# Performance work log

Measured on AMD Instinct MI355X. Metric: run time of the kernel, lower is better.

## Reference

```python
import jax, jax.numpy as jnp
import numpy as np


def setup_inputs() -> dict:
    key = jax.random.key(0)
    k1, k2, k3 = jax.random.split(key, 3)
    B, C, S, Fin, Fout = 16, 64, 2048, 64, 64
    x = jax.random.normal(k1, (B, C, S, Fin), dtype=jnp.float32)
    # positive entries so row sums are > 0 and sqrt is well-defined
    adj = jax.random.uniform(k2, (C, C), dtype=jnp.float32)
    weight = jax.random.normal(k3, (Fin, Fout), dtype=jnp.float32) * (1.0 / np.sqrt(Fin))
    return {"x": x, "adj": adj, "weight": weight}


def reference(x, adj, weight):
    # Symmetric normalization: D^{-1/2} A D^{-1/2}. The torch code builds a
    # full diag + matrix inverse; mathematically this is elementwise rsqrt
    # row/col scaling of adj.
    d_inv_sqrt = jax.lax.rsqrt(jnp.sum(adj, axis=1))          # [C]
    norm_adj = adj * d_inv_sqrt[:, None] * d_inv_sqrt[None, :]  # [C, C]
    # support[b,c,s,o] = sum_f x[b,c,s,f] * weight[f,o]
    support = jnp.einsum('bcsf,fo->bcso', x, weight)
    # mix over channel (graph node) dim: out[b,c,s,o] = sum_d A_norm[c,d] support[b,d,s,o]
    out = jnp.einsum('cd,bdso->bcso', norm_adj, support)
    return jax.nn.relu(out)
```

## Files before the change

kernel.cpp:

```cpp
#include <hip/hip_runtime.h>
#include <hip/hip_bf16.h>

#define B_ 16
#define C_ 64
#define S_ 2048
#define F_ 64
#define SF (S_ * F_)

typedef __attribute__((ext_vector_type(8))) short short8;
typedef __attribute__((ext_vector_type(4))) float float4_;

#define SWZ(row, col) ((col) ^ (((row) & 7) << 3))

__device__ __forceinline__ unsigned short f2bf(float f) {
    unsigned int u = __builtin_bit_cast(unsigned int, f);
    u += 0x7fffu + ((u >> 16) & 1u);
    return (unsigned short)(u >> 16);
}

__global__ void gcn_prep(const float* __restrict__ adj, const float* __restrict__ wgt,
                         unsigned short* __restrict__ nadj, unsigned short* __restrict__ wT)
{
    __shared__ float dis[C_];
    const int t = threadIdx.x;
    if (t < C_) {
        float s = 0.f;
        for (int d = 0; d < C_; ++d) s += adj[t * C_ + d];
        dis[t] = rsqrtf(s);
    }
    __syncthreads();
    for (int i = t; i < C_ * C_; i += 256) {
        const int c = i >> 6, d = i & 63;
        nadj[i] = f2bf(adj[i] * dis[c] * dis[d]);
        wT[d * F_ + c] = f2bf(wgt[i]);
    }
}

__global__ __launch_bounds__(512, 4) void gcn_main(
    const float* __restrict__ x,
    const unsigned short* __restrict__ nadj,
    const unsigned short* __restrict__ wT,
    float* __restrict__ out)
{
    __shared__ __align__(16) unsigned short lds_nadj[C_ * C_];
    __shared__ __align__(16) unsigned short lds_wT[F_ * F_];
    __shared__ __align__(16) unsigned short supT[8 * 16 * F_];

    const int tid  = threadIdx.x;
    const int w    = tid >> 6;
    const int l    = tid & 63;
    const int lrow = l & 15;
    const int lgrp = l >> 4;

    {
        const int fc = tid >> 3;
        const int fd = (tid & 7) * 8;
        *(short8*)(lds_nadj + fc * 64 + SWZ(fc, fd)) = *(const short8*)(nadj + fc * 64 + fd);
        *(short8*)(lds_wT  + fc * 64 + SWZ(fc, fd)) = *(const short8*)(wT  + fc * 64 + fd);
    }
    __syncthreads();

    const int b  = blockIdx.x >> 8;
    const int st = blockIdx.x & 255;
    const int s  = st * 8 + w;

    const float* xb = x + (size_t)b * C_ * SF + (size_t)s * F_;
    short8 af[4][2];
#pragma unroll
    for (int dt = 0; dt < 4; ++dt) {
        const float* xr = xb + (size_t)(dt * 16 + lrow) * SF;
#pragma unroll
        for (int ks = 0; ks < 2; ++ks) {
            float4_ u0 = *(const float4_*)(xr + ks * 32 + lgrp * 8);
            float4_ u1 = *(const float4_*)(xr + ks * 32 + lgrp * 8 + 4);
            short8 a;
#pragma unroll
            for (int j = 0; j < 4; ++j) {
                a[j]     = (short)f2bf(u0[j]);
                a[4 + j] = (short)f2bf(u1[j]);
            }
            af[dt][ks] = a;
        }
    }

    unsigned short* myT = supT + w * (16 * F_);
    float* ob = out + (size_t)b * C_ * SF + (size_t)s * F_;

#pragma unroll
    for (int ot = 0; ot < 4; ++ot) {
        const int orow = ot * 16 + lrow;
        short8 wf0 = *(const short8*)(lds_wT + orow * 64 + SWZ(lrow, lgrp * 8));
        short8 wf1 = *(const short8*)(lds_wT + orow * 64 + SWZ(lrow, 32 + lgrp * 8));

#pragma unroll
        for (int dt = 0; dt < 4; ++dt) {
            float4_ s1 = {0.f, 0.f, 0.f, 0.f};
            s1 = __builtin_amdgcn_mfma_f32_16x16x32_bf16(af[dt][0], wf0, s1, 0, 0, 0);
            s1 = __builtin_amdgcn_mfma_f32_16x16x32_bf16(af[dt][1], wf1, s1, 0, 0, 0);
            const int dbase = dt * 16 + lgrp * 4;
            uint2 pk;
            pk.x = (unsigned)f2bf(s1[0]) | ((unsigned)f2bf(s1[1]) << 16);
            pk.y = (unsigned)f2bf(s1[2]) | ((unsigned)f2bf(s1[3]) << 16);
            *(uint2*)(myT + lrow * 64 + SWZ(lrow, dbase)) = pk;
        }

        short8 bf0 = *(const short8*)(myT + lrow * 64 + SWZ(lrow, lgrp * 8));
        short8 bf1 = *(const short8*)(myT + lrow * 64 + SWZ(lrow, 32 + lgrp * 8));

#pragma unroll
        for (int ct = 0; ct < 4; ++ct) {
            const int crow = ct * 16 + lrow;
            short8 an0 = *(const short8*)(lds_nadj + crow * 64 + SWZ(lrow, lgrp * 8));
            short8 an1 = *(const short8*)(lds_nadj + crow * 64 + SWZ(lrow, 32 + lgrp * 8));
            float4_ acc = {0.f, 0.f, 0.f, 0.f};
            acc = __builtin_amdgcn_mfma_f32_16x16x32_bf16(bf0, an0, acc, 0, 0, 0);
            acc = __builtin_amdgcn_mfma_f32_16x16x32_bf16(bf1, an1, acc, 0, 0, 0);
            float4_ r;
#pragma unroll
            for (int i = 0; i < 4; ++i) r[i] = fmaxf(acc[i], 0.f);
            *(float4_*)(ob + (size_t)crow * SF + ot * 16 + lgrp * 4) = r;
        }
    }
}

extern "C" void kernel_launch(void* const* d_in, const int* in_sizes, int n_in,
                              void* d_out, int out_size, void* d_ws, size_t ws_size,
                              hipStream_t stream) {
    const float* x   = (const float*)d_in[0];
    const float* adj = (const float*)d_in[1];
    const float* wgt = (const float*)d_in[2];
    float* out = (float*)d_out;

    unsigned short* nadj = (unsigned short*)d_ws;
    unsigned short* wT   = nadj + C_ * C_;

    gcn_prep<<<1, 256, 0, stream>>>(adj, wgt, nadj, wT);

    dim3 grid(B_ * (S_ / 8));
    gcn_main<<<grid, 512, 0, stream>>>(x, nadj, wT, out);
}
```

Baseline: 253.5 us.

## Loop each wave over multiple positions with double-buffered nontemporal x loads

Restructures the main kernel so each 256-thread block processes 32 sequence positions, with each wave looping over 8 of them. Register double-buffering prefetches the next x slab during the MFMA work. Loads and stores use nontemporal hints, and output stores are paired into adjacent segments. The aim is to hide global-memory latency and amortise LDS setup across more work, at the cost of more register pressure and fewer resident waves.

```diff
diff --git a/kernel.cpp b/kernel.cpp
--- a/kernel.cpp
+++ b/kernel.cpp
@@ -6,6 +6,7 @@
 #define S_ 2048
 #define F_ 64
 #define SF (S_ * F_)
+#define NS 8
 
 typedef __attribute__((ext_vector_type(8))) short short8;
 typedef __attribute__((ext_vector_type(4))) float float4_;
@@ -16,6 +17,16 @@
     unsigned int u = __builtin_bit_cast(unsigned int, f);
     u += 0x7fffu + ((u >> 16) & 1u);
     return (unsigned short)(u >> 16);
+}
+
+__device__ __forceinline__ short8 pack8(float4_ u0, float4_ u1) {
+    short8 a;
+#pragma unroll
+    for (int j = 0; j < 4; ++j) {
+        a[j]     = (short)f2bf(u0[j]);
+        a[4 + j] = (short)f2bf(u1[j]);
+    }
+    return a;
 }
 
 __global__ void gcn_prep(const float* __restrict__ adj, const float* __restrict__ wgt,
@@ -36,7 +47,21 @@
     }
 }
 
-__global__ __launch_bounds__(512, 4) void gcn_main(
+__device__ __forceinline__ void load_half(float4_ (&R)[2][2][2], const float* xit,
+                                          const int dtbase, const int lrow, const int lgrp)
+{
+#pragma unroll
+    for (int dd = 0; dd < 2; ++dd) {
+        const float* xr = xit + (size_t)((dtbase + dd) * 16 + lrow) * SF;
+#pragma unroll
+        for (int ks = 0; ks < 2; ++ks) {
+            R[dd][ks][0] = __builtin_nontemporal_load((const float4_*)(xr + ks * 32 + lgrp * 8));
+            R[dd][ks][1] = __builtin_nontemporal_load((const float4_*)(xr + ks * 32 + lgrp * 8 + 4));
+        }
+    }
+}
+
+__global__ __launch_bounds__(256, 3) void gcn_main(
     const float* __restrict__ x,
     const unsigned short* __restrict__ nadj,
     const unsigned short* __restrict__ wT,
@@ -44,7 +69,7 @@
 {
     __shared__ __align__(16) unsigned short lds_nadj[C_ * C_];
     __shared__ __align__(16) unsigned short lds_wT[F_ * F_];
-    __shared__ __align__(16) unsigned short supT[8 * 16 * F_];
+    __shared__ __align__(16) unsigned short supT[4 * 16 * F_];
 
     const int tid  = threadIdx.x;
     const int w    = tid >> 6;
@@ -53,73 +78,90 @@
     const int lgrp = l >> 4;
 
     {
-        const int fc = tid >> 3;
-        const int fd = (tid & 7) * 8;
-        *(short8*)(lds_nadj + fc * 64 + SWZ(fc, fd)) = *(const short8*)(nadj + fc * 64 + fd);
-        *(short8*)(lds_wT  + fc * 64 + SWZ(fc, fd)) = *(const short8*)(wT  + fc * 64 + fd);
+        const int fc = tid >> 2;
+        const int fd = (tid & 3) * 16;
+        *(short8*)(lds_nadj + fc * 64 + SWZ(fc, fd))     = *(const short8*)(nadj + fc * 64 + fd);
+        *(short8*)(lds_nadj + fc * 64 + SWZ(fc, fd + 8)) = *(const short8*)(nadj + fc * 64 + fd + 8);
+        *(short8*)(lds_wT  + fc * 64 + SWZ(fc, fd))      = *(const short8*)(wT  + fc * 64 + fd);
+        *(short8*)(lds_wT  + fc * 64 + SWZ(fc, fd + 8))  = *(const short8*)(wT  + fc * 64 + fd + 8);
     }
     __syncthreads();
 
-    const int b  = blockIdx.x >> 8;
-    const int st = blockIdx.x & 255;
-    const int s  = st * 8 + w;
+    const int b     = blockIdx.x >> 6;
+    const int chunk = blockIdx.x & 63;
+    const float* xbase = x   + (size_t)b * C_ * SF + (size_t)(chunk * 32 + w) * F_;
+    float*       obase = out + (size_t)b * C_ * SF + (size_t)(chunk * 32 + w) * F_;
+    unsigned short* myT = supT + w * (16 * F_);
 
-    const float* xb = x + (size_t)b * C_ * SF + (size_t)s * F_;
-    short8 af[4][2];
+    float4_ rA[2][2][2], rB[2][2][2];
+    load_half(rA, xbase, 0, lrow, lgrp);
+    load_half(rB, xbase, 2, lrow, lgrp);
+
+#pragma unroll 1
+    for (int i = 0; i < NS; ++i) {
+        short8 af[4][2];
 #pragma unroll
-    for (int dt = 0; dt < 4; ++dt) {
-        const float* xr = xb + (size_t)(dt * 16 + lrow) * SF;
+        for (int dd = 0; dd < 2; ++dd)
 #pragma unroll
-        for (int ks = 0; ks < 2; ++ks) {
-            float4_ u0 = *(const float4_*)(xr + ks * 32 + lgrp * 8);
-            float4_ u1 = *(const float4_*)(xr + ks * 32 + lgrp * 8 + 4);
-            short8 a;
-#pragma unroll
-            for (int j = 0; j < 4; ++j) {
-                a[j]     = (short)f2bf(u0[j]);
-                a[4 + j] = (short)f2bf(u1[j]);
+            for (int ks = 0; ks < 2; ++ks) {
+                af[dd][ks]     = pack8(rA[dd][ks][0], rA[dd][ks][1]);
+                af[2 + dd][ks] = pack8(rB[dd][ks][0], rB[dd][ks][1]);
             }
-            af[dt][ks] = a;
-        }
-    }
 
-    unsigned short* myT = supT + w * (16 * F_);
-    float* ob = out + (size_t)b * C_ * SF + (size_t)s * F_;
+        const float* xnext = xbase + (size_t)(i + 1) * (4 * F_);
+        float* ob = obase + (size_t)i * (4 * F_);
+
+        if (i + 1 < NS) load_half(rA, xnext, 0, lrow, lgrp);
+
+        float4_ keep[4];
+
+        auto do_ot = [&](const int ot) {
+            const int orow = ot * 16 + lrow;
+            short8 wf0 = *(const short8*)(lds_wT + orow * 64 + SWZ(lrow, lgrp * 8));
+            short8 wf1 = *(const short8*)(lds_wT + orow * 64 + SWZ(lrow, 32 + lgrp * 8));
 
 #pragma unroll
-    for (int ot = 0; ot < 4; ++ot) {
-        const int orow = ot * 16 + lrow;
-        short8 wf0 = *(const short8*)(lds_wT + orow * 64 + SWZ(lrow, lgrp * 8));
-        short8 wf1 = *(const short8*)(lds_wT + orow * 64 + SWZ(lrow, 32 + lgrp * 8));
+            for (int dt = 0; dt < 4; ++dt) {
+                float4_ s1 = {0.f, 0.f, 0.f, 0.f};
+                s1 = __builtin_amdgcn_mfma_f32_16x16x32_bf16(af[dt][0], wf0, s1, 0, 0, 0);
+                s1 = __builtin_amdgcn_mfma_f32_16x16x32_bf16(af[dt][1], wf1, s1, 0, 0, 0);
+                const int dbase = dt * 16 + lgrp * 4;
+                uint2 pk;
+                pk.x = (unsigned)f2bf(s1[0]) | ((unsigned)f2bf(s1[1]) << 16);
+                pk.y = (unsigned)f2bf(s1[2]) | ((unsigned)f2bf(s1[3]) << 16);
+                *(uint2*)(myT + lrow * 64 + SWZ(lrow, dbase)) = pk;
+            }
+
+            short8 bf0 = *(const short8*)(myT + lrow * 64 + SWZ(lrow, lgrp * 8));
+            short8 bf1 = *(const short8*)(myT + lrow * 64 + SWZ(lrow, 32 + lgrp * 8));
 
 #pragma unroll
-        for (int dt = 0; dt < 4; ++dt) {
-            float4_ s1 = {0.f, 0.f, 0.f, 0.f};
-            s1 = __builtin_amdgcn_mfma_f32_16x16x32_bf16(af[dt][0], wf0, s1, 0, 0, 0);
-            s1 = __builtin_amdgcn_mfma_f32_16x16x32_bf16(af[dt][1], wf1, s1, 0, 0, 0);
-            const int dbase = dt * 16 + lgrp * 4;
-            uint2 pk;
-            pk.x = (unsigned)f2bf(s1[0]) | ((unsigned)f2bf(s1[1]) << 16);
-            pk.y = (unsigned)f2bf(s1[2]) | ((unsigned)f2bf(s1[3]) << 16);
-            *(uint2*)(myT + lrow * 64 + SWZ(lrow, dbase)) = pk;
-        }
+            for (int ct = 0; ct < 4; ++ct) {
+                const int crow = ct * 16 + lrow;
+                short8 an0 = *(const short8*)(lds_nadj + crow * 64 + SWZ(lrow, lgrp * 8));
+                short8 an1 = *(const short8*)(lds_nadj + crow * 64 + SWZ(lrow, 32 + lgrp * 8));
+                float4_ acc = {0.f, 0.f, 0.f, 0.f};
+                acc = __builtin_amdgcn_mfma_f32_16x16x32_bf16(bf0, an0, acc, 0, 0, 0);
+                acc = __builtin_amdgcn_mfma_f32_16x16x32_bf16(bf1, an1, acc, 0, 0, 0);
+                float4_ r;
+#pragma unroll
+                for (int j = 0; j < 4; ++j) r[j] = fmaxf(acc[j], 0.f);
+                if (ot & 1) {
+                    __builtin_nontemporal_store(keep[ct],
+                        (float4_*)(ob + (size_t)crow * SF + (ot - 1) * 16 + lgrp * 4));
+                    __builtin_nontemporal_store(r,
+                        (float4_*)(ob + (size_t)crow * SF + ot * 16 + lgrp * 4));
+                } else {
+                    keep[ct] = r;
+                }
+            }
+        };
 
-        short8 bf0 = *(const short8*)(myT + lrow * 64 + SWZ(lrow, lgrp * 8));
-        short8 bf1 = *(const short8*)(myT + lrow * 64 + SWZ(lrow, 32 + lgrp * 8));
-
-#pragma unroll
-        for (int ct = 0; ct < 4; ++ct) {
-            const int crow = ct * 16 + lrow;
-            short8 an0 = *(const short8*)(lds_nadj + crow * 64 + SWZ(lrow, lgrp * 8));
-            short8 an1 = *(const short8*)(lds_nadj + crow * 64 + SWZ(lrow, 32 + lgrp * 8));
-            float4_ acc = {0.f, 0.f, 0.f, 0.f};
-            acc = __builtin_amdgcn_mfma_f32_16x16x32_bf16(bf0, an0, acc, 0, 0, 0);
-            acc = __builtin_amdgcn_mfma_f32_16x16x32_bf16(bf1, an1, acc, 0, 0, 0);
-            float4_ r;
-#pragma unroll
-            for (int i = 0; i < 4; ++i) r[i] = fmaxf(acc[i], 0.f);
-            *(float4_*)(ob + (size_t)crow * SF + ot * 16 + lgrp * 4) = r;
-        }
+        do_ot(0);
+        do_ot(1);
+        if (i + 1 < NS) load_half(rB, xnext, 2, lrow, lgrp);
+        do_ot(2);
+        do_ot(3);
     }
 }
 
@@ -136,6 +178,6 @@
 
     gcn_prep<<<1, 256, 0, stream>>>(adj, wgt, nadj, wT);
 
-    dim3 grid(B_ * (S_ / 8));
-    gcn_main<<<grid, 512, 0, stream>>>(x, nadj, wT, out);
+    dim3 grid(B_ * (S_ / 32));
+    gcn_main<<<grid, 256, 0, stream>>>(x, nadj, wT, out);
 }
```

Measured after the change: 372.3 us. 1.47x slower.

## Process output tiles in pairs to reuse adjacency fragments and add nontemporal loads

Applied to the files above, without the earlier changes.

The per-wave loop over output-feature tiles now handles two tiles per iteration. Support for both tiles is staged in a doubled per-wave LDS buffer, so each pair of normalized-adjacency fragments loaded from LDS serves two MFMA chains instead of one. x is read with nontemporal loads to avoid polluting the cache, and launch bounds are raised to request six blocks per CU. The doubled supT buffer raises LDS use per block, which may cap occupancy below the new target, and the extra live fragments add register pressure.

```diff
diff --git a/kernel.cpp b/kernel.cpp
--- a/kernel.cpp
+++ b/kernel.cpp
@@ -36,7 +36,7 @@
     }
 }
 
-__global__ __launch_bounds__(512, 4) void gcn_main(
+__global__ __launch_bounds__(512, 6) void gcn_main(
     const float* __restrict__ x,
     const unsigned short* __restrict__ nadj,
     const unsigned short* __restrict__ wT,
@@ -44,7 +44,7 @@
 {
     __shared__ __align__(16) unsigned short lds_nadj[C_ * C_];
     __shared__ __align__(16) unsigned short lds_wT[F_ * F_];
-    __shared__ __align__(16) unsigned short supT[8 * 16 * F_];
+    __shared__ __align__(16) unsigned short supT[8 * 32 * F_];
 
     const int tid  = threadIdx.x;
     const int w    = tid >> 6;
@@ -71,8 +71,8 @@
         const float* xr = xb + (size_t)(dt * 16 + lrow) * SF;
 #pragma unroll
         for (int ks = 0; ks < 2; ++ks) {
-            float4_ u0 = *(const float4_*)(xr + ks * 32 + lgrp * 8);
-            float4_ u1 = *(const float4_*)(xr + ks * 32 + lgrp * 8 + 4);
+            float4_ u0 = __builtin_nontemporal_load((const float4_*)(xr + ks * 32 + lgrp * 8));
+            float4_ u1 = __builtin_nontemporal_load((const float4_*)(xr + ks * 32 + lgrp * 8 + 4));
             short8 a;
 #pragma unroll
             for (int j = 0; j < 4; ++j) {
@@ -83,42 +83,58 @@
         }
     }
 
-    unsigned short* myT = supT + w * (16 * F_);
+    unsigned short* myT = supT + w * (32 * F_);
     float* ob = out + (size_t)b * C_ * SF + (size_t)s * F_;
 
+#pragma unroll 1
+    for (int p = 0; p < 2; ++p) {
 #pragma unroll
-    for (int ot = 0; ot < 4; ++ot) {
-        const int orow = ot * 16 + lrow;
-        short8 wf0 = *(const short8*)(lds_wT + orow * 64 + SWZ(lrow, lgrp * 8));
-        short8 wf1 = *(const short8*)(lds_wT + orow * 64 + SWZ(lrow, 32 + lgrp * 8));
-
+        for (int par = 0; par < 2; ++par) {
+            const int ot = 2 * p + par;
+            const int orow = ot * 16 + lrow;
+            short8 wf0 = *(const short8*)(lds_wT + orow * 64 + SWZ(lrow, lgrp * 8));
+            short8 wf1 = *(const short8*)(lds_wT + orow * 64 + SWZ(lrow, 32 + lgrp * 8));
+            unsigned short* tT = myT + par * (16 * F_);
 #pragma unroll
-        for (int dt = 0; dt < 4; ++dt) {
-            float4_ s1 = {0.f, 0.f, 0.f, 0.f};
-            s1 = __builtin_amdgcn_mfma_f32_16x16x32_bf16(af[dt][0], wf0, s1, 0, 0, 0);
-            s1 = __builtin_amdgcn_mfma_f32_16x16x32_bf16(af[dt][1], wf1, s1, 0, 0, 0);
-            const int dbase = dt * 16 + lgrp * 4;
-            uint2 pk;
-            pk.x = (unsigned)f2bf(s1[0]) | ((unsigned)f2bf(s1[1]) << 16);
-            pk.y = (unsigned)f2bf(s1[2]) | ((unsigned)f2bf(s1[3]) << 16);
-            *(uint2*)(myT + lrow * 64 + SWZ(lrow, dbase)) = pk;
+            for (int dt = 0; dt < 4; ++dt) {
+                float4_ s1 = {0.f, 0.f, 0.f, 0.f};
+                s1 = __builtin_amdgcn_mfma_f32_16x16x32_bf16(af[dt][0], wf0, s1, 0, 0, 0);
+                s1 = __builtin_amdgcn_mfma_f32_16x16x32_bf16(af[dt][1], wf1, s1, 0, 0, 0);
+                const int dbase = dt * 16 + lgrp * 4;
+                uint2 pk;
+                pk.x = (unsigned)f2bf(s1[0]) | ((unsigned)f2bf(s1[1]) << 16);
+                pk.y = (unsigned)f2bf(s1[2]) | ((unsigned)f2bf(s1[3]) << 16);
+                *(uint2*)(tT + lrow * 64 + SWZ(lrow, dbase)) = pk;
+            }
         }
 
-        short8 bf0 = *(const short8*)(myT + lrow * 64 + SWZ(lrow, lgrp * 8));
-        short8 bf1 = *(const short8*)(myT + lrow * 64 + SWZ(lrow, 32 + lgrp * 8));
+        short8 be0 = *(const short8*)(myT + lrow * 64 + SWZ(lrow, lgrp * 8));
+        short8 be1 = *(const short8*)(myT + lrow * 64 + SWZ(lrow, 32 + lgrp * 8));
+        short8 bo0 = *(const short8*)(myT + (16 * F_) + lrow * 64 + SWZ(lrow, lgrp * 8));
+        short8 bo1 = *(const short8*)(myT + (16 * F_) + lrow * 64 + SWZ(lrow, 32 + lgrp * 8));
 
 #pragma unroll
         for (int ct = 0; ct < 4; ++ct) {
             const int crow = ct * 16 + lrow;
             short8 an0 = *(const short8*)(lds_nadj + crow * 64 + SWZ(lrow, lgrp * 8));
             short8 an1 = *(const short8*)(lds_nadj + crow * 64 + SWZ(lrow, 32 + lgrp * 8));
-            float4_ acc = {0.f, 0.f, 0.f, 0.f};
-            acc = __builtin_amdgcn_mfma_f32_16x16x32_bf16(bf0, an0, acc, 0, 0, 0);
-            acc = __builtin_amdgcn_mfma_f32_16x16x32_bf16(bf1, an1, acc, 0, 0, 0);
-            float4_ r;
+
+            float4_ ae = {0.f, 0.f, 0.f, 0.f};
+            ae = __builtin_amdgcn_mfma_f32_16x16x32_bf16(be0, an0, ae, 0, 0, 0);
+            ae = __builtin_amdgcn_mfma_f32_16x16x32_bf16(be1, an1, ae, 0, 0, 0);
+            float4_ ao = {0.f, 0.f, 0.f, 0.f};
+            ao = __builtin_amdgcn_mfma_f32_16x16x32_bf16(bo0, an0, ao, 0, 0, 0);
+            ao = __builtin_amdgcn_mfma_f32_16x16x32_bf16(bo1, an1, ao, 0, 0, 0);
+
+            float4_ re, ro;
 #pragma unroll
-            for (int i = 0; i < 4; ++i) r[i] = fmaxf(acc[i], 0.f);
-            *(float4_*)(ob + (size_t)crow * SF + ot * 16 + lgrp * 4) = r;
+            for (int j = 0; j < 4; ++j) {
+                re[j] = fmaxf(ae[j], 0.f);
+                ro[j] = fmaxf(ao[j], 0.f);
+            }
+            float* dst = ob + (size_t)crow * SF + p * 32 + lgrp * 4;
+            *(float4_*)(dst)      = re;
+            *(float4_*)(dst + 16) = ro;
         }
     }
 }
```

After: 353.4 us. 39.4% more time.

## Stage output tile in LDS for contiguous nontemporal stores and reorder loops

Applied to the files above, without the earlier changes.

Reorders the second GEMM so each channel tile is finished across all output features, then stages the relu results in a swizzled LDS buffer. The block writes contiguous 2KB rows to global memory with nontemporal stores instead of scattered 64-byte pieces per wave. It also switches the x loads to nontemporal. The cost is an LDS buffer that grows from 16KB to 32KB plus extra block-wide barriers, which may reduce occupancy and add synchronization stalls.

```diff
diff --git a/kernel.cpp b/kernel.cpp
--- a/kernel.cpp
+++ b/kernel.cpp
@@ -44,7 +44,7 @@
 {
     __shared__ __align__(16) unsigned short lds_nadj[C_ * C_];
     __shared__ __align__(16) unsigned short lds_wT[F_ * F_];
-    __shared__ __align__(16) unsigned short supT[8 * 16 * F_];
+    __shared__ __align__(16) unsigned char u_mem[32768];
 
     const int tid  = threadIdx.x;
     const int w    = tid >> 6;
@@ -71,8 +71,8 @@
         const float* xr = xb + (size_t)(dt * 16 + lrow) * SF;
 #pragma unroll
         for (int ks = 0; ks < 2; ++ks) {
-            float4_ u0 = *(const float4_*)(xr + ks * 32 + lgrp * 8);
-            float4_ u1 = *(const float4_*)(xr + ks * 32 + lgrp * 8 + 4);
+            float4_ u0 = __builtin_nontemporal_load((const float4_*)(xr + ks * 32 + lgrp * 8));
+            float4_ u1 = __builtin_nontemporal_load((const float4_*)(xr + ks * 32 + lgrp * 8 + 4));
             short8 a;
 #pragma unroll
             for (int j = 0; j < 4; ++j) {
@@ -83,15 +83,15 @@
         }
     }
 
-    unsigned short* myT = supT + w * (16 * F_);
-    float* ob = out + (size_t)b * C_ * SF + (size_t)s * F_;
+    unsigned short* myT = (unsigned short*)u_mem + w * (16 * F_);
+    float* obuf = (float*)u_mem;
 
+    short8 aA[4][2];
 #pragma unroll
     for (int ot = 0; ot < 4; ++ot) {
         const int orow = ot * 16 + lrow;
         short8 wf0 = *(const short8*)(lds_wT + orow * 64 + SWZ(lrow, lgrp * 8));
         short8 wf1 = *(const short8*)(lds_wT + orow * 64 + SWZ(lrow, 32 + lgrp * 8));
-
 #pragma unroll
         for (int dt = 0; dt < 4; ++dt) {
             float4_ s1 = {0.f, 0.f, 0.f, 0.f};
@@ -103,23 +103,40 @@
             pk.y = (unsigned)f2bf(s1[2]) | ((unsigned)f2bf(s1[3]) << 16);
             *(uint2*)(myT + lrow * 64 + SWZ(lrow, dbase)) = pk;
         }
+        aA[ot][0] = *(const short8*)(myT + lrow * 64 + SWZ(lrow, lgrp * 8));
+        aA[ot][1] = *(const short8*)(myT + lrow * 64 + SWZ(lrow, 32 + lgrp * 8));
+    }
+    __syncthreads();
 
-        short8 bf0 = *(const short8*)(myT + lrow * 64 + SWZ(lrow, lgrp * 8));
-        short8 bf1 = *(const short8*)(myT + lrow * 64 + SWZ(lrow, 32 + lgrp * 8));
+#pragma unroll 1
+    for (int ct = 0; ct < 4; ++ct) {
+        const int crow = ct * 16 + lrow;
+        short8 an0 = *(const short8*)(lds_nadj + crow * 64 + SWZ(lrow, lgrp * 8));
+        short8 an1 = *(const short8*)(lds_nadj + crow * 64 + SWZ(lrow, 32 + lgrp * 8));
+#pragma unroll
+        for (int ot = 0; ot < 4; ++ot) {
+            float4_ acc = {0.f, 0.f, 0.f, 0.f};
+            acc = __builtin_amdgcn_mfma_f32_16x16x32_bf16(aA[ot][0], an0, acc, 0, 0, 0);
+            acc = __builtin_amdgcn_mfma_f32_16x16x32_bf16(aA[ot][1], an1, acc, 0, 0, 0);
+            float4_ r;
+#pragma unroll
+            for (int j = 0; j < 4; ++j) r[j] = fmaxf(acc[j], 0.f);
+            const int col = w * 64 + ot * 16 + lgrp * 4;
+            *(float4_*)(obuf + lrow * 512 + (col ^ ((lrow & 7) * 4))) = r;
+        }
+        __syncthreads();
 
 #pragma unroll
-        for (int ct = 0; ct < 4; ++ct) {
-            const int crow = ct * 16 + lrow;
-            short8 an0 = *(const short8*)(lds_nadj + crow * 64 + SWZ(lrow, lgrp * 8));
-            short8 an1 = *(const short8*)(lds_nadj + crow * 64 + SWZ(lrow, 32 + lgrp * 8));
-            float4_ acc = {0.f, 0.f, 0.f, 0.f};
-            acc = __builtin_amdgcn_mfma_f32_16x16x32_bf16(bf0, an0, acc, 0, 0, 0);
-            acc = __builtin_amdgcn_mfma_f32_16x16x32_bf16(bf1, an1, acc, 0, 0, 0);
-            float4_ r;
-#pragma unroll
-            for (int i = 0; i < 4; ++i) r[i] = fmaxf(acc[i], 0.f);
-            *(float4_*)(ob + (size_t)crow * SF + ot * 16 + lgrp * 4) = r;
+        for (int t = 0; t < 4; ++t) {
+            const int task = w * 4 + t;
+            const int cl    = task >> 1;
+            const int half  = task & 1;
+            const int col   = half * 256 + l * 4;
+            float4_ v = *(const float4_*)(obuf + cl * 512 + (col ^ ((cl & 7) * 4)));
+            float* g = out + (((size_t)(b * C_ + ct * 16 + cl) * S_ + st * 8) * F_) + col;
+            __builtin_nontemporal_store(v, (float4_*)g);
         }
+        if (ct < 3) __syncthreads();
     }
 }
 
```

Result: faster. 219.2 us (-13.5%).
